# Performance work log

Hardware: AMD Instinct MI355X
Metric: run time of the kernel (lower is better)

## Reference

```python
import jax, jax.numpy as jnp
import numpy as np

B, LQ, LK = 4, 128, 1024
Q_SIZE, K_SIZE, V_SIZE, UNITS = 512, 512, 512, 256
MASK_VAL = -1e6  # matches torch masked_softmax value=-1000000.0


def setup_inputs() -> dict:
    key = jax.random.key(0)
    ks = jax.random.split(key, 7)
    return {
        "query": jax.random.normal(ks[0], (B, LQ, Q_SIZE), dtype=jnp.float32),
        "key": jax.random.normal(ks[1], (B, LK, K_SIZE), dtype=jnp.float32),
        "value": jax.random.normal(ks[2], (B, LK, V_SIZE), dtype=jnp.float32),
        "valid_len": jax.random.randint(ks[3], (B,), 1, LK + 1).astype(jnp.int64),
        # torch nn.Linear(in, out, bias=False) weight is (out, in)
        "W_q": jax.random.normal(ks[4], (UNITS, Q_SIZE), dtype=jnp.float32) / np.sqrt(Q_SIZE),
        "W_k": jax.random.normal(ks[5], (UNITS, K_SIZE), dtype=jnp.float32) / np.sqrt(K_SIZE),
        "v": jax.random.normal(ks[6], (UNITS,), dtype=jnp.float32) / np.sqrt(UNITS),
    }


def reference(query, key, value, valid_len, W_q, W_k, v):
    # projections: (B,Lq,units), (B,Lk,units)
    q = jnp.einsum("bqd,ud->bqu", query, W_q)
    k = jnp.einsum("bkd,ud->bku", key, W_k)
    # additive features: (B,Lq,Lk,units)
    feats = jnp.tanh(q[:, :, None, :] + k[:, None, :, :])
    # v-projection -> scores (B,Lq,Lk)
    scores = jnp.einsum("bqku,u->bqk", feats, v)
    # mask positions >= valid_len with -1e6 (same as torch sequence_mask)
    mask = jnp.arange(scores.shape[-1]) < valid_len[:, None, None]
    scores = jnp.where(mask, scores, MASK_VAL)
    attn = jax.nn.softmax(scores, axis=-1)  # dropout rate is 0.0
    return jnp.einsum("bqk,bkv->bqv", attn, value)
```

## Files before the change

### kernel.cpp

```cpp
#include <hip/hip_runtime.h>


typedef _Float16 half8 __attribute__((ext_vector_type(8)));
typedef float floatx4 __attribute__((ext_vector_type(4)));

#define EQ_OFF   0
#define EKT_OFF  (512 * 256)

__global__ __launch_bounds__(256) void proj_mfma(
    const float* __restrict__ query, const float* __restrict__ key,
    const float* __restrict__ W_q, const float* __restrict__ W_k,
    const int* __restrict__ vlen, float* __restrict__ Eq,
    float* __restrict__ EkT) {
  __shared__ __align__(16) _Float16 As[64 * 32];
  __shared__ __align__(16) _Float16 Bs[64 * 32];
  const int tid = threadIdx.x;
  const int mb = blockIdx.x;
  const int u0 = blockIdx.y * 64;
  const bool qpart = mb < 8;
  const float *Ag, *Bg;
  int kbatch = 0, j0 = 0, m0 = 0;
  if (qpart) {
    m0 = mb * 64;
    Ag = query + (size_t)m0 * 512;
    Bg = W_q + (size_t)u0 * 512;
  } else {
    const int g0 = (mb - 8) * 64;
    kbatch = g0 >> 10;
    j0 = g0 & 1023;
    if (j0 >= vlen[kbatch]) return;
    Ag = W_k + (size_t)u0 * 512;
    Bg = key + (size_t)g0 * 512;
  }

  const int lrow = tid >> 2, lkq = (tid & 3) * 8;
  const float* Ags = Ag + lrow * 512 + lkq;
  const float* Bgs = Bg + lrow * 512 + lkq;
  _Float16* Ads = As + lrow * 32 + lkq;
  _Float16* Bds = Bs + lrow * 32 + lkq;

  const int lane = tid & 63;
  const int wid = tid >> 6;
  const int wm = (wid & 1) * 32, wn = (wid >> 1) * 32;
  const int frow = lane & 15;
  const int fk = (lane >> 4) * 8;

  floatx4 acc[2][2] = {{{0.f, 0.f, 0.f, 0.f}, {0.f, 0.f, 0.f, 0.f}},
                       {{0.f, 0.f, 0.f, 0.f}, {0.f, 0.f, 0.f, 0.f}}};

  float4 ra0 = *(const float4*)Ags;
  float4 ra1 = *(const float4*)(Ags + 4);
  float4 rb0 = *(const float4*)Bgs;
  float4 rb1 = *(const float4*)(Bgs + 4);

  for (int kb = 0; kb < 16; ++kb) {
    half8 ha, hb;
    ha[0] = (_Float16)ra0.x; ha[1] = (_Float16)ra0.y;
    ha[2] = (_Float16)ra0.z; ha[3] = (_Float16)ra0.w;
    ha[4] = (_Float16)ra1.x; ha[5] = (_Float16)ra1.y;
    ha[6] = (_Float16)ra1.z; ha[7] = (_Float16)ra1.w;
    hb[0] = (_Float16)rb0.x; hb[1] = (_Float16)rb0.y;
    hb[2] = (_Float16)rb0.z; hb[3] = (_Float16)rb0.w;
    hb[4] = (_Float16)rb1.x; hb[5] = (_Float16)rb1.y;
    hb[6] = (_Float16)rb1.z; hb[7] = (_Float16)rb1.w;
    __syncthreads();
    *(half8*)Ads = ha;
    *(half8*)Bds = hb;
    __syncthreads();
    if (kb + 1 < 16) {
      ra0 = *(const float4*)(Ags + (kb + 1) * 32);
      ra1 = *(const float4*)(Ags + (kb + 1) * 32 + 4);
      rb0 = *(const float4*)(Bgs + (kb + 1) * 32);
      rb1 = *(const float4*)(Bgs + (kb + 1) * 32 + 4);
    }
    half8 a0 = *(const half8*)(As + (wm + frow) * 32 + fk);
    half8 a1 = *(const half8*)(As + (wm + 16 + frow) * 32 + fk);
    half8 b0 = *(const half8*)(Bs + (wn + frow) * 32 + fk);
    half8 b1 = *(const half8*)(Bs + (wn + 16 + frow) * 32 + fk);
    acc[0][0] = __builtin_amdgcn_mfma_f32_16x16x32_f16(a0, b0, acc[0][0], 0, 0, 0);
    acc[0][1] = __builtin_amdgcn_mfma_f32_16x16x32_f16(a0, b1, acc[0][1], 0, 0, 0);
    acc[1][0] = __builtin_amdgcn_mfma_f32_16x16x32_f16(a1, b0, acc[1][0], 0, 0, 0);
    acc[1][1] = __builtin_amdgcn_mfma_f32_16x16x32_f16(a1, b1, acc[1][1], 0, 0, 0);
  }

  const int rbase = (lane >> 4) * 4;
  const int col = lane & 15;
#pragma unroll
  for (int mi = 0; mi < 2; ++mi)
#pragma unroll
    for (int ni = 0; ni < 2; ++ni)
#pragma unroll
      for (int r = 0; r < 4; ++r) {
        const int R = wm + mi * 16 + rbase + r;
        const int C = wn + ni * 16 + col;
        const float e = __expf(2.f * acc[mi][ni][r]);
        if (qpart)
          Eq[(m0 + R) * 256 + u0 + C] = e;
        else
          EkT[kbatch * 262144 + (u0 + R) * 1024 + j0 + C] = e;
      }
}

__global__ __launch_bounds__(1024) void scores_attn(
    const float* __restrict__ Eq, const float* __restrict__ EkT,
    const float* __restrict__ vvec, const int* __restrict__ valid_len,
    const float* __restrict__ value, float* __restrict__ out) {
  __shared__ float4 QV[256];
  __shared__ float P0[1024];
  __shared__ float P1[1024];
  __shared__ float2 red[16];
  __shared__ float4 red2[8][2][128];
  const int tid = threadIdx.x;
  const int b = blockIdx.x >> 6;
  const int i0 = (blockIdx.x & 63) * 2;
  const int vl = valid_len[b];

  float vv = 0.f;
  if (tid < 256) {
    vv = vvec[tid];
    QV[tid] = make_float4(Eq[(b * 128 + i0) * 256 + tid],
                          Eq[(b * 128 + i0 + 1) * 256 + tid], -2.f * vv, 0.f);
  }
  float sv = vv;
#pragma unroll
  for (int off = 32; off > 0; off >>= 1) sv += __shfl_xor(sv, off, 64);
  if ((tid & 63) == 0) red[tid >> 6] = make_float2(sv, 0.f);
  __syncthreads();
  float SV = 0.f;
#pragma unroll
  for (int w = 0; w < 16; ++w) SV += red[w].x;

  const int j = tid;
  float p0 = 0.f, p1 = 0.f;
  if (j < vl) {
    float a0 = 0.f, a1 = 0.f;
    const float* kp = EkT + b * 262144 + j;
#pragma unroll 8
    for (int u = 0; u < 256; ++u) {
      float ek = kp[u << 10];
      float4 q = QV[u];
      float r0 = __builtin_amdgcn_rcpf(fmaf(q.x, ek, 1.f));
      float r1 = __builtin_amdgcn_rcpf(fmaf(q.y, ek, 1.f));
      a0 = fmaf(q.z, r0, a0);
      a1 = fmaf(q.z, r1, a1);
    }
    p0 = __expf(SV + a0);
    p1 = __expf(SV + a1);
  }
  P0[j] = p0;
  P1[j] = p1;

  float2 pp = make_float2(p0, p1);
#pragma unroll
  for (int off = 32; off > 0; off >>= 1) {
    pp.x += __shfl_xor(pp.x, off, 64);
    pp.y += __shfl_xor(pp.y, off, 64);
  }
  __syncthreads();
  if ((tid & 63) == 0) red[tid >> 6] = pp;
  __syncthreads();
  float den0 = 0.f, den1 = 0.f;
#pragma unroll
  for (int w = 0; w < 16; ++w) { den0 += red[w].x; den1 += red[w].y; }

  const int cg = tid & 127;
  const int jq = tid >> 7;
  const float* Vb = value + b * 524288 + cg * 4;
  float4 acc0 = make_float4(0.f, 0.f, 0.f, 0.f);
  float4 acc1 = make_float4(0.f, 0.f, 0.f, 0.f);
  const int js = jq * 128;
  const int je = min(js + 128, vl);
  for (int j4 = js; j4 < je; j4 += 4) {
    float4 q0 = *(const float4*)(P0 + j4);
    float4 q1 = *(const float4*)(P1 + j4);
#pragma unroll
    for (int t = 0; t < 4; ++t) {
      float4 v4 = *(const float4*)(Vb + (j4 + t) * 512);
      float w0 = t == 0 ? q0.x : t == 1 ? q0.y : t == 2 ? q0.z : q0.w;
      float w1 = t == 0 ? q1.x : t == 1 ? q1.y : t == 2 ? q1.z : q1.w;
      acc0.x = fmaf(w0, v4.x, acc0.x); acc0.y = fmaf(w0, v4.y, acc0.y);
      acc0.z = fmaf(w0, v4.z, acc0.z); acc0.w = fmaf(w0, v4.w, acc0.w);
      acc1.x = fmaf(w1, v4.x, acc1.x); acc1.y = fmaf(w1, v4.y, acc1.y);
      acc1.z = fmaf(w1, v4.z, acc1.z); acc1.w = fmaf(w1, v4.w, acc1.w);
    }
  }
  red2[jq][0][cg] = acc0;
  red2[jq][1][cg] = acc1;
  __syncthreads();

  if (tid < 256) {
    const int r = tid >> 7, cg2 = tid & 127;
    float4 s = make_float4(0.f, 0.f, 0.f, 0.f);
#pragma unroll
    for (int q = 0; q < 8; ++q) {
      float4 x = red2[q][r][cg2];
      s.x += x.x; s.y += x.y; s.z += x.z; s.w += x.w;
    }
    const float rden = __builtin_amdgcn_rcpf(r ? den1 : den0);
    s.x *= rden; s.y *= rden; s.z *= rden; s.w *= rden;
    *(float4*)(out + (b * 128 + i0 + r) * 512 + cg2 * 4) = s;
  }
}

extern "C" void kernel_launch(void* const* d_in, const int* in_sizes, int n_in,
                              void* d_out, int out_size, void* d_ws, size_t ws_size,
                              hipStream_t stream) {
  const float* query = (const float*)d_in[0];
  const float* key   = (const float*)d_in[1];
  const float* value = (const float*)d_in[2];
  const int*   vlen  = (const int*)d_in[3];
  const float* W_q   = (const float*)d_in[4];
  const float* W_k   = (const float*)d_in[5];
  const float* v     = (const float*)d_in[6];
  float* out = (float*)d_out;

  float* ws  = (float*)d_ws;
  float* Eq  = ws + EQ_OFF;
  float* EkT = ws + EKT_OFF;

  proj_mfma<<<dim3(72, 4), 256, 0, stream>>>(query, key, W_q, W_k, vlen, Eq, EkT);
  scores_attn<<<256, 1024, 0, stream>>>(Eq, EkT, v, vlen, value, out);
}
```

Before: 113.5 us.

## Split score reduction over units, vectorize key loads, double-buffer projection LDS

Result: slower. 116.3 us (+2.5%).

```diff
diff --git a/kernel.cpp b/kernel.cpp
--- a/kernel.cpp
+++ b/kernel.cpp
@@ -12,8 +12,8 @@
     const float* __restrict__ W_q, const float* __restrict__ W_k,
     const int* __restrict__ vlen, float* __restrict__ Eq,
     float* __restrict__ EkT) {
-  __shared__ __align__(16) _Float16 As[64 * 32];
-  __shared__ __align__(16) _Float16 Bs[64 * 32];
+  __shared__ __align__(16) _Float16 As[2][64 * 32];
+  __shared__ __align__(16) _Float16 Bs[2][64 * 32];
   const int tid = threadIdx.x;
   const int mb = blockIdx.x;
   const int u0 = blockIdx.y * 64;
@@ -36,8 +36,7 @@
   const int lrow = tid >> 2, lkq = (tid & 3) * 8;
   const float* Ags = Ag + lrow * 512 + lkq;
   const float* Bgs = Bg + lrow * 512 + lkq;
-  _Float16* Ads = As + lrow * 32 + lkq;
-  _Float16* Bds = Bs + lrow * 32 + lkq;
+  const int lofs = lrow * 32 + lkq;
 
   const int lane = tid & 63;
   const int wid = tid >> 6;
@@ -54,6 +53,7 @@
   float4 rb1 = *(const float4*)(Bgs + 4);
 
   for (int kb = 0; kb < 16; ++kb) {
+    const int buf = kb & 1;
     half8 ha, hb;
     ha[0] = (_Float16)ra0.x; ha[1] = (_Float16)ra0.y;
     ha[2] = (_Float16)ra0.z; ha[3] = (_Float16)ra0.w;
@@ -63,9 +63,8 @@
     hb[2] = (_Float16)rb0.z; hb[3] = (_Float16)rb0.w;
     hb[4] = (_Float16)rb1.x; hb[5] = (_Float16)rb1.y;
     hb[6] = (_Float16)rb1.z; hb[7] = (_Float16)rb1.w;
-    __syncthreads();
-    *(half8*)Ads = ha;
-    *(half8*)Bds = hb;
+    *(half8*)(As[buf] + lofs) = ha;
+    *(half8*)(Bs[buf] + lofs) = hb;
     __syncthreads();
     if (kb + 1 < 16) {
       ra0 = *(const float4*)(Ags + (kb + 1) * 32);
@@ -73,10 +72,10 @@
       rb0 = *(const float4*)(Bgs + (kb + 1) * 32);
       rb1 = *(const float4*)(Bgs + (kb + 1) * 32 + 4);
     }
-    half8 a0 = *(const half8*)(As + (wm + frow) * 32 + fk);
-    half8 a1 = *(const half8*)(As + (wm + 16 + frow) * 32 + fk);
-    half8 b0 = *(const half8*)(Bs + (wn + frow) * 32 + fk);
-    half8 b1 = *(const half8*)(Bs + (wn + 16 + frow) * 32 + fk);
+    half8 a0 = *(const half8*)(As[buf] + (wm + frow) * 32 + fk);
+    half8 a1 = *(const half8*)(As[buf] + (wm + 16 + frow) * 32 + fk);
+    half8 b0 = *(const half8*)(Bs[buf] + (wn + frow) * 32 + fk);
+    half8 b1 = *(const half8*)(Bs[buf] + (wn + 16 + frow) * 32 + fk);
     acc[0][0] = __builtin_amdgcn_mfma_f32_16x16x32_f16(a0, b0, acc[0][0], 0, 0, 0);
     acc[0][1] = __builtin_amdgcn_mfma_f32_16x16x32_f16(a0, b1, acc[0][1], 0, 0, 0);
     acc[1][0] = __builtin_amdgcn_mfma_f32_16x16x32_f16(a1, b0, acc[1][0], 0, 0, 0);
@@ -105,14 +104,15 @@
     const float* __restrict__ Eq, const float* __restrict__ EkT,
     const float* __restrict__ vvec, const int* __restrict__ valid_len,
     const float* __restrict__ value, float* __restrict__ out) {
-  __shared__ float4 QV[256];
-  __shared__ float P0[1024];
-  __shared__ float P1[1024];
+  __shared__ __align__(16) float4 QV[256];
+  __shared__ __align__(16) float part[4][2][1024];
+  __shared__ __align__(16) float P0[1024], P1[1024];
   __shared__ float2 red[16];
-  __shared__ float4 red2[8][2][128];
+  __shared__ __align__(16) float4 red2[8][2][128];
   const int tid = threadIdx.x;
-  const int b = blockIdx.x >> 6;
-  const int i0 = (blockIdx.x & 63) * 2;
+  const int bx = blockIdx.x;
+  const int b = (bx >> 1) & 3;
+  const int i0 = ((((bx >> 3) << 1) | (bx & 1))) * 2;
   const int vl = valid_len[b];
 
   float vv = 0.f;
@@ -130,25 +130,40 @@
 #pragma unroll
   for (int w = 0; w < 16; ++w) SV += red[w].x;
 
-  const int j = tid;
-  float p0 = 0.f, p1 = 0.f;
-  if (j < vl) {
-    float a0 = 0.f, a1 = 0.f;
-    const float* kp = EkT + b * 262144 + j;
-#pragma unroll 8
-    for (int u = 0; u < 256; ++u) {
-      float ek = kp[u << 10];
-      float4 q = QV[u];
-      float r0 = __builtin_amdgcn_rcpf(fmaf(q.x, ek, 1.f));
-      float r1 = __builtin_amdgcn_rcpf(fmaf(q.y, ek, 1.f));
-      a0 = fmaf(q.z, r0, a0);
-      a1 = fmaf(q.z, r1, a1);
-    }
-    p0 = __expf(SV + a0);
-    p1 = __expf(SV + a1);
-  }
-  P0[j] = p0;
-  P1[j] = p1;
+  const int uq = tid >> 8;
+  const int j4 = (tid & 255) * 4;
+  float4 acc0 = make_float4(0.f, 0.f, 0.f, 0.f);
+  float4 acc1 = make_float4(0.f, 0.f, 0.f, 0.f);
+  if (j4 < vl) {
+    const float* kp = EkT + b * 262144 + (uq << 16) + j4;
+#pragma unroll 4
+    for (int u = 0; u < 64; ++u) {
+      float4 ek = *(const float4*)(kp + (u << 10));
+      float4 q = QV[(uq << 6) + u];
+      float r00 = __builtin_amdgcn_rcpf(fmaf(q.x, ek.x, 1.f));
+      float r01 = __builtin_amdgcn_rcpf(fmaf(q.x, ek.y, 1.f));
+      float r02 = __builtin_amdgcn_rcpf(fmaf(q.x, ek.z, 1.f));
+      float r03 = __builtin_amdgcn_rcpf(fmaf(q.x, ek.w, 1.f));
+      float r10 = __builtin_amdgcn_rcpf(fmaf(q.y, ek.x, 1.f));
+      float r11 = __builtin_amdgcn_rcpf(fmaf(q.y, ek.y, 1.f));
+      float r12 = __builtin_amdgcn_rcpf(fmaf(q.y, ek.z, 1.f));
+      float r13 = __builtin_amdgcn_rcpf(fmaf(q.y, ek.w, 1.f));
+      acc0.x = fmaf(q.z, r00, acc0.x); acc0.y = fmaf(q.z, r01, acc0.y);
+      acc0.z = fmaf(q.z, r02, acc0.z); acc0.w = fmaf(q.z, r03, acc0.w);
+      acc1.x = fmaf(q.z, r10, acc1.x); acc1.y = fmaf(q.z, r11, acc1.y);
+      acc1.z = fmaf(q.z, r12, acc1.z); acc1.w = fmaf(q.z, r13, acc1.w);
+    }
+  }
+  *(float4*)&part[uq][0][j4] = acc0;
+  *(float4*)&part[uq][1][j4] = acc1;
+  __syncthreads();
+
+  float s0 = part[0][0][tid] + part[1][0][tid] + part[2][0][tid] + part[3][0][tid];
+  float s1 = part[0][1][tid] + part[1][1][tid] + part[2][1][tid] + part[3][1][tid];
+  float p0 = (tid < vl) ? __expf(SV + s0) : 0.f;
+  float p1 = (tid < vl) ? __expf(SV + s1) : 0.f;
+  P0[tid] = p0;
+  P1[tid] = p1;
 
   float2 pp = make_float2(p0, p1);
 #pragma unroll
@@ -156,7 +171,6 @@
     pp.x += __shfl_xor(pp.x, off, 64);
     pp.y += __shfl_xor(pp.y, off, 64);
   }
-  __syncthreads();
   if ((tid & 63) == 0) red[tid >> 6] = pp;
   __syncthreads();
   float den0 = 0.f, den1 = 0.f;
@@ -166,26 +180,26 @@
   const int cg = tid & 127;
   const int jq = tid >> 7;
   const float* Vb = value + b * 524288 + cg * 4;
-  float4 acc0 = make_float4(0.f, 0.f, 0.f, 0.f);
-  float4 acc1 = make_float4(0.f, 0.f, 0.f, 0.f);
+  float4 acc0b = make_float4(0.f, 0.f, 0.f, 0.f);
+  float4 acc1b = make_float4(0.f, 0.f, 0.f, 0.f);
   const int js = jq * 128;
   const int je = min(js + 128, vl);
-  for (int j4 = js; j4 < je; j4 += 4) {
-    float4 q0 = *(const float4*)(P0 + j4);
-    float4 q1 = *(const float4*)(P1 + j4);
+  for (int jj = js; jj < je; jj += 4) {
+    float4 q0 = *(const float4*)(P0 + jj);
+    float4 q1 = *(const float4*)(P1 + jj);
 #pragma unroll
     for (int t = 0; t < 4; ++t) {
-      float4 v4 = *(const float4*)(Vb + (j4 + t) * 512);
+      float4 v4 = *(const float4*)(Vb + (jj + t) * 512);
       float w0 = t == 0 ? q0.x : t == 1 ? q0.y : t == 2 ? q0.z : q0.w;
       float w1 = t == 0 ? q1.x : t == 1 ? q1.y : t == 2 ? q1.z : q1.w;
-      acc0.x = fmaf(w0, v4.x, acc0.x); acc0.y = fmaf(w0, v4.y, acc0.y);
-      acc0.z = fmaf(w0, v4.z, acc0.z); acc0.w = fmaf(w0, v4.w, acc0.w);
-      acc1.x = fmaf(w1, v4.x, acc1.x); acc1.y = fmaf(w1, v4.y, acc1.y);
-      acc1.z = fmaf(w1, v4.z, acc1.z); acc1.w = fmaf(w1, v4.w, acc1.w);
-    }
-  }
-  red2[jq][0][cg] = acc0;
-  red2[jq][1][cg] = acc1;
+      acc0b.x = fmaf(w0, v4.x, acc0b.x); acc0b.y = fmaf(w0, v4.y, acc0b.y);
+      acc0b.z = fmaf(w0, v4.z, acc0b.z); acc0b.w = fmaf(w0, v4.w, acc0b.w);
+      acc1b.x = fmaf(w1, v4.x, acc1b.x); acc1b.y = fmaf(w1, v4.y, acc1b.y);
+      acc1b.z = fmaf(w1, v4.z, acc1b.z); acc1b.w = fmaf(w1, v4.w, acc1b.w);
+    }
+  }
+  red2[jq][0][cg] = acc0b;
+  red2[jq][1][cg] = acc1b;
   __syncthreads();
 
   if (tid < 256) {
```
